# Kernel optimization log

Hardware: AMD Instinct MI355X
Metric: run time of the kernel (lower is better)

## Reference

```python
import jax, jax.numpy as jnp
import numpy as np
from jax import lax

B, T, D, H = 4, 2048, 1024, 8
DH = D // H          # head dim
K = 4                # causal conv kernel
DFF = int(D * 4 / 3) # 1365, GLU up-projection
EPS_LN = 1e-5
EPS_SLSTM = 1e-8


def layernorm(x, g, b):
    mu = jnp.mean(x, axis=-1, keepdims=True)
    var = jnp.mean(jnp.square(x - mu), axis=-1, keepdims=True)
    return (x - mu) * lax.rsqrt(var + EPS_LN) * g + b


def bd(x, W):
    # block-diagonal linear: x [..., D], W [H, DH, DH]
    xh = x.reshape(x.shape[:-1] + (H, DH))
    return jnp.einsum('...hd,hde->...he', xh, W).reshape(x.shape)


def _forward(x, Wz, Wi, Wf, Wo, bz, bi, bf, bo, Rz, Ri, Rf, Ro,
             conv_w, conv_b, ln_g, ln_b, gn_g, gn_b,
             left_w, left_b, right_w, right_b, last_w, last_b):
    x_norm = layernorm(x, ln_g, ln_b)
    # causal conv1d (pad left K-1), NCH layout
    xc = x_norm.transpose(0, 2, 1)
    conv = lax.conv_general_dilated(xc, conv_w, (1,), [(K - 1, 0)],
                                    dimension_numbers=('NCH', 'OIH', 'NCH'))
    conv = conv + conv_b[None, :, None]
    x_if = conv.transpose(0, 2, 1)
    x_if = x_if * jax.nn.sigmoid(x_if)  # swish (dropout = identity in eval)
    x_zo = x_norm

    # precompute input-side block-diagonal projections for all timesteps
    wz = bd(x_zo, Wz) + bz
    wi = bd(x_if, Wi) + bi
    wf = bd(x_if, Wf) + bf
    wo = bd(x_zo, Wo) + bo

    zeros = jnp.zeros((B, D), x.dtype)

    def step(carry, inp):
        h, c, n, m = carry
        wz_t, wi_t, wf_t, wo_t = inp
        z_bar = wz_t + bd(h, Rz)
        i_bar = wi_t + bd(h, Ri)
        f_bar = wf_t + bd(h, Rf)
        o_bar = wo_t + bd(h, Ro)
        z = jnp.tanh(z_bar)
        o = jax.nn.sigmoid(o_bar)
        m_next = jnp.maximum(f_bar + m, i_bar)
        i = jnp.exp(i_bar - m_next)
        f = jnp.exp(f_bar + m - m_next)
        c_next = f * c + i * z
        n_next = f * n + i
        h_next = o * (c_next / jnp.maximum(jnp.abs(n_next), EPS_SLSTM))
        return (h_next, c_next, n_next, m_next), h_next

    seq = (wz.transpose(1, 0, 2), wi.transpose(1, 0, 2),
           wf.transpose(1, 0, 2), wo.transpose(1, 0, 2))
    (h, c, n, m), hs = lax.scan(step, (zeros, zeros, zeros, zeros), seq)
    h_seq = hs.transpose(1, 0, 2)  # [B, T, D]

    h_gn = layernorm(h_seq, gn_g, gn_b)
    h_skip = h_gn + x
    hn = layernorm(h_skip, ln_g, ln_b)  # shared ln params, as in the module
    z_left = hn @ left_w.T + left_b
    z_right = jax.nn.gelu(hn @ right_w.T + right_b, approximate=False)
    out = (z_left * z_right) @ last_w.T + last_b + h_skip
    return out, h, c, n, m


def setup_inputs() -> dict:
    key = jax.random.key(0)
    ks = jax.random.split(key, 16)
    s = 0.02
    nrm = lambda k, shape: jax.random.normal(k, shape, jnp.float32) * s
    return dict(
        x=jax.random.normal(ks[0], (B, T, D), jnp.float32),
        Wz=nrm(ks[1], (H, DH, DH)), Wi=nrm(ks[2], (H, DH, DH)),
        Wf=nrm(ks[3], (H, DH, DH)), Wo=nrm(ks[4], (H, DH, DH)),
        bz=jnp.zeros(D), bi=jnp.zeros(D), bf=jnp.zeros(D), bo=jnp.zeros(D),
        Rz=nrm(ks[5], (H, DH, DH)), Ri=nrm(ks[6], (H, DH, DH)),
        Rf=nrm(ks[7], (H, DH, DH)), Ro=nrm(ks[8], (H, DH, DH)),
        conv_w=nrm(ks[9], (D, D, K)), conv_b=jnp.zeros(D),
        ln_g=jnp.ones(D), ln_b=jnp.zeros(D),
        gn_g=jnp.ones(D), gn_b=jnp.zeros(D),
        left_w=nrm(ks[10], (DFF, D)), left_b=jnp.zeros(DFF),
        right_w=nrm(ks[11], (DFF, D)), right_b=jnp.zeros(DFF),
        last_w=nrm(ks[12], (D, DFF)), last_b=jnp.zeros(D),
    )


def reference(x, Wz, Wi, Wf, Wo, bz, bi, bf, bo, Rz, Ri, Rf, Ro,
              conv_w, conv_b, ln_g, ln_b, gn_g, gn_b,
              left_w, left_b, right_w, right_b, last_w, last_b):
    out, h, c, n, m = _forward(x, Wz, Wi, Wf, Wo, bz, bi, bf, bo,
                               Rz, Ri, Rf, Ro, conv_w, conv_b,
                               ln_g, ln_b, gn_g, gn_b,
                               left_w, left_b, right_w, right_b,
                               last_w, last_b)
    return (out, (h, c, n, m))
```

## Files before the change

kernel.cpp:

```cpp
#include <hip/hip_runtime.h>

typedef unsigned short u16;
typedef unsigned int u32;
typedef __attribute__((ext_vector_type(8))) short short8;
typedef __attribute__((ext_vector_type(4))) float f32x4;

#define B_  4
#define T_  2048
#define D_  1024
#define H_  8
#define DH_ 128
#define DFF_ 1365
#define DFFP 1408
#define NLR 2816

__device__ __forceinline__ u16 f2bf(float f) {
    u32 u = __float_as_uint(f);
    u32 r = (u + 0x7fffu + ((u >> 16) & 1u)) >> 16;
    return (u16)r;
}
__device__ __forceinline__ float bf2f(u16 v) {
    return __uint_as_float(((u32)v) << 16);
}
__device__ __forceinline__ float frcp(float x) { return __builtin_amdgcn_rcpf(x); }

__global__ void ln_x_kernel(const float* __restrict__ x, const float* __restrict__ g,
                            const float* __restrict__ b, u16* __restrict__ xn) {
    int row = blockIdx.x, tid = threadIdx.x;
    int lane = tid & 63, wv = tid >> 6;
    __shared__ float red[8];
    float4 v = ((const float4*)(x + (size_t)row * D_))[tid];
    float s = v.x + v.y + v.z + v.w;
    float s2 = v.x * v.x + v.y * v.y + v.z * v.z + v.w * v.w;
#pragma unroll
    for (int o = 32; o >= 1; o >>= 1) { s += __shfl_xor(s, o); s2 += __shfl_xor(s2, o); }
    if (lane == 0) { red[wv] = s; red[4 + wv] = s2; }
    __syncthreads();
    s = red[0] + red[1] + red[2] + red[3];
    s2 = red[4] + red[5] + red[6] + red[7];
    float mu = s * (1.f / D_);
    float var = s2 * (1.f / D_) - mu * mu;
    float inv = rsqrtf(var + 1e-5f);
    int c0 = tid * 4;
    ushort4 o4;
    o4.x = f2bf((v.x - mu) * inv * g[c0 + 0] + b[c0 + 0]);
    o4.y = f2bf((v.y - mu) * inv * g[c0 + 1] + b[c0 + 1]);
    o4.z = f2bf((v.z - mu) * inv * g[c0 + 2] + b[c0 + 2]);
    o4.w = f2bf((v.w - mu) * inv * g[c0 + 3] + b[c0 + 3]);
    ((ushort4*)(xn + (size_t)row * D_))[tid] = o4;
}

__global__ void build_bconv2(const float* __restrict__ cw, u16* __restrict__ oh,
                             u16* __restrict__ ol) {
    int i = blockIdx.x * 256 + threadIdx.x;
    int din = i & 1023, kt = (i >> 10) & 3, dout = i >> 12;
    float v = cw[((size_t)dout * D_ + din) * 4 + kt];
    u16 hi = f2bf(v);
    oh[i] = hi;
    ol[i] = f2bf(v - bf2f(hi));
}

__global__ __launch_bounds__(256) void proj2_kernel(
    const u16* __restrict__ xn, const float* __restrict__ xif,
    const float* __restrict__ Wz, const float* __restrict__ Wi,
    const float* __restrict__ Wf, const float* __restrict__ Wo,
    const float* __restrict__ bz, const float* __restrict__ bi,
    const float* __restrict__ bfv, const float* __restrict__ bo,
    float* __restrict__ wgif, u16* __restrict__ wgzo) {
    const int m0 = blockIdx.x * 32;
    const int hd = blockIdx.y;
    const int tid = threadIdx.x;
    const int e = tid & 127, half = tid >> 7;
    __shared__ float xns[32][128];
    __shared__ float xfs[32][128];
    for (int s = tid; s < 32 * 128; s += 256) {
        int r = s >> 7, d = s & 127;
        xns[r][d] = bf2f(xn[(size_t)(m0 + r) * D_ + hd * DH_ + d]);
        xfs[r][d] = xif[(size_t)(m0 + r) * D_ + hd * DH_ + d];
    }
    __syncthreads();
    const float* WA = half ? Wo : Wz;
    const float* WB = half ? Wf : Wi;
    float accA[32], accB[32];
#pragma unroll
    for (int r = 0; r < 32; ++r) { accA[r] = 0.f; accB[r] = 0.f; }
    for (int d = 0; d < 128; ++d) {
        float wa = WA[((size_t)hd * DH_ + d) * DH_ + e];
        float wb = WB[((size_t)hd * DH_ + d) * DH_ + e];
#pragma unroll
        for (int r = 0; r < 32; ++r) {
            accA[r] += xns[r][d] * wa;
            accB[r] += xfs[r][d] * wb;
        }
    }
    float ba = half ? bo[hd * DH_ + e] : bz[hd * DH_ + e];
    float bb = half ? bfv[hd * DH_ + e] : bi[hd * DH_ + e];
#pragma unroll
    for (int r = 0; r < 32; ++r) {
        size_t base = ((size_t)(m0 + r) * D_ + hd * DH_ + e) * 2;
        wgif[base + half] = accB[r] + bb;
        wgzo[base + half] = f2bf(accA[r] + ba);
    }
}

__global__ void build_blr(const float* __restrict__ lw, const float* __restrict__ rw,
                          u16* __restrict__ o) {
    int i = blockIdx.x * 256 + threadIdx.x;
    int k = i & 1023, n = i >> 10;
    float v = 0.f;
    if (n < DFF_) v = lw[(size_t)n * D_ + k];
    else if (n >= DFFP && n < DFFP + DFF_) v = rw[(size_t)(n - DFFP) * D_ + k];
    o[i] = f2bf(v);
}
__global__ void build_blast(const float* __restrict__ lw, u16* __restrict__ o) {
    int n = blockIdx.x;
    for (int k = threadIdx.x; k < DFFP; k += 256) {
        float v = (k < DFF_) ? lw[(size_t)n * DFF_ + k] : 0.f;
        o[(size_t)n * DFFP + k] = f2bf(v);
    }
}

template <int MODE>
__global__ __launch_bounds__(256) void gemm_k(
    const u16* __restrict__ A, const u16* __restrict__ Bg, const u16* __restrict__ Bg2,
    int K, int lda,
    const float* __restrict__ bias0, const float* __restrict__ bias1,
    const float* __restrict__ add0, u16* __restrict__ o16, float* __restrict__ o32) {
    const int tid = threadIdx.x;
    const int m0 = blockIdx.y * 128;
    const int n0 = blockIdx.x * 128;
    __shared__ u16 As[128][72];
    __shared__ u16 Bs[128][72];
    __shared__ u16 Bs2[(MODE == 0) ? 128 : 1][72];

    f32x4 zero4 = {0.f, 0.f, 0.f, 0.f};
    f32x4 acc[4][4];
#pragma unroll
    for (int i = 0; i < 4; ++i)
#pragma unroll
        for (int j = 0; j < 4; ++j) acc[i][j] = zero4;

    const int lane = tid & 63, wv = tid >> 6;
    const int wr = (wv >> 1) * 64, wc = (wv & 1) * 64;
    const int fr = lane & 15, kg = (lane >> 4) * 8;

    for (int kb = 0; kb < K; kb += 64) {
#pragma unroll
        for (int it = 0; it < 4; ++it) {
            int slot = tid + it * 256;
            int r = slot >> 3, ch = slot & 7;
            uint4 va;
            if constexpr (MODE == 0) {
                int kk = kb + ch * 8;
                int ktap = kk >> 10, din = kk & 1023;
                int m = m0 + r;
                int t = m & (T_ - 1);
                if (t + ktap - 3 >= 0)
                    va = *(const uint4*)(A + (size_t)(m + ktap - 3) * D_ + din);
                else
                    va = make_uint4(0u, 0u, 0u, 0u);
            } else {
                va = *(const uint4*)(A + (size_t)(m0 + r) * lda + kb + ch * 8);
            }
            *(uint4*)(&As[r][ch * 8]) = va;
            uint4 vb = *(const uint4*)(Bg + (size_t)(n0 + r) * K + kb + ch * 8);
            *(uint4*)(&Bs[r][ch * 8]) = vb;
            if constexpr (MODE == 0) {
                uint4 vc = *(const uint4*)(Bg2 + (size_t)(n0 + r) * K + kb + ch * 8);
                *(uint4*)(&Bs2[r][ch * 8]) = vc;
            }
        }
        __syncthreads();
#pragma unroll
        for (int kt = 0; kt < 2; ++kt) {
            short8 af[4], bfr[4];
#pragma unroll
            for (int i = 0; i < 4; ++i)
                af[i] = *(const short8*)(&As[wr + i * 16 + fr][kt * 32 + kg]);
#pragma unroll
            for (int i = 0; i < 4; ++i)
                bfr[i] = *(const short8*)(&Bs[wc + i * 16 + fr][kt * 32 + kg]);
#pragma unroll
            for (int mi = 0; mi < 4; ++mi)
#pragma unroll
                for (int ni = 0; ni < 4; ++ni)
                    acc[mi][ni] = __builtin_amdgcn_mfma_f32_16x16x32_bf16(
                        af[mi], bfr[ni], acc[mi][ni], 0, 0, 0);
            if constexpr (MODE == 0) {
                short8 bl[4];
#pragma unroll
                for (int i = 0; i < 4; ++i)
                    bl[i] = *(const short8*)(&Bs2[wc + i * 16 + fr][kt * 32 + kg]);
#pragma unroll
                for (int mi = 0; mi < 4; ++mi)
#pragma unroll
                    for (int ni = 0; ni < 4; ++ni)
                        acc[mi][ni] = __builtin_amdgcn_mfma_f32_16x16x32_bf16(
                            af[mi], bl[ni], acc[mi][ni], 0, 0, 0);
            }
        }
        __syncthreads();
    }
#pragma unroll
    for (int mi = 0; mi < 4; ++mi) {
#pragma unroll
        for (int ni = 0; ni < 4; ++ni) {
#pragma unroll
            for (int r = 0; r < 4; ++r) {
                int row = m0 + wr + mi * 16 + (lane >> 4) * 4 + r;
                int col = n0 + wc + ni * 16 + fr;
                float v = acc[mi][ni][r];
                if constexpr (MODE == 0) {
                    float s = v + bias0[col];
                    float sw = s * frcp(1.f + __expf(-s));
                    o32[(size_t)row * D_ + col] = sw;
                } else if constexpr (MODE == 2) {
                    float bv = 0.f;
                    if (col < DFF_) bv = bias0[col];
                    else if (col >= DFFP && col < DFFP + DFF_) bv = bias1[col - DFFP];
                    o16[(size_t)row * NLR + col] = f2bf(v + bv);
                } else {
                    float r0 = v + bias0[col] + add0[(size_t)row * D_ + col];
                    o32[(size_t)row * D_ + col] = r0;
                }
            }
        }
    }
}

__global__ __launch_bounds__(512) void scan4_kernel(
    const float* __restrict__ wgif, const u16* __restrict__ wgzo,
    const float* __restrict__ Rz, const float* __restrict__ Ri,
    const float* __restrict__ Rf, const float* __restrict__ Ro,
    u16* __restrict__ hseq, float* __restrict__ st_out) {
    const int head = blockIdx.x;
    const int tid = threadIdx.x;
    const int lane = tid & 63, wv = tid >> 6;
    const int lc = lane & 15, lg = lane >> 4;

    __shared__ u16 hfH[2][4][64][8];
    __shared__ u16 hfL[2][4][64][8];
    __shared__ float zl[8][4][16][4];

    for (int i = tid; i < 2 * 4 * 64 * 8; i += 512) {
        ((u16*)hfH)[i] = 0;
        ((u16*)hfL)[i] = 0;
    }

    short8 bfh[4][4];
    short8 bfl[2][4];
    {
        const float* Rp[4] = {Rz, Ri, Rf, Ro};
        const int e = wv * 16 + lc;
#pragma unroll
        for (int g = 0; g < 4; ++g) {
            const float* R = Rp[g] + (size_t)head * DH_ * DH_;
#pragma unroll
            for (int kt = 0; kt < 4; ++kt) {
                short8 vh, vl;
#pragma unroll
                for (int j = 0; j < 8; ++j) {
                    int k = kt * 32 + lg * 8 + j;
                    float rv = R[(size_t)k * DH_ + e];
                    u16 hi = f2bf(rv);
                    vh[j] = (short)hi;
                    vl[j] = (short)f2bf(rv - bf2f(hi));
                }
                bfh[g][kt] = vh;
                if (g == 1) bfl[0][kt] = vl;
                if (g == 2) bfl[1][kt] = vl;
            }
        }
    }

    const int ab = lg;
    const int adq = wv * 16 + lc;
    const float* pifp = wgif + (((size_t)ab * T_) * D_ + head * DH_ + adq) * 2;
    const u16*  pzop = wgzo + (((size_t)ab * T_) * D_ + head * DH_ + adq) * 2;
    u16* hsp = hseq + ((size_t)ab * T_) * D_ + head * DH_ + adq;
    const int fpos = (((adq >> 5) * 64) + (((adq >> 3) & 3) * 16) + ab) * 8 + (adq & 7);
    const bool ard = (lc < 4);

    float c_s = 0.f, n_s = 0.f, m_s = 0.f, h_s = 0.f;
    float2 pif = *(const float2*)pifp; pifp += 2 * D_;
    u32 pzo = *(const u32*)pzop; pzop += 2 * D_;

    const short8 zero8 = {0, 0, 0, 0, 0, 0, 0, 0};
    __syncthreads();

    for (int t = 0; t < T_; ++t) {
        const int p = t & 1, q = p ^ 1;
        short8 ah[4], al[4];
#pragma unroll
        for (int kt = 0; kt < 4; ++kt) {
            ah[kt] = ard ? *(const short8*)(&hfH[p][kt][lane][0]) : zero8;
            al[kt] = ard ? *(const short8*)(&hfL[p][kt][lane][0]) : zero8;
        }
        f32x4 az = {0.f, 0.f, 0.f, 0.f}, ai = az, af2 = az, ao = az;
#pragma unroll
        for (int kt = 0; kt < 4; ++kt) {
            az  = __builtin_amdgcn_mfma_f32_16x16x32_bf16(ah[kt], bfh[0][kt], az, 0, 0, 0);
            ao  = __builtin_amdgcn_mfma_f32_16x16x32_bf16(ah[kt], bfh[3][kt], ao, 0, 0, 0);
            ai  = __builtin_amdgcn_mfma_f32_16x16x32_bf16(ah[kt], bfh[1][kt], ai, 0, 0, 0);
            af2 = __builtin_amdgcn_mfma_f32_16x16x32_bf16(ah[kt], bfh[2][kt], af2, 0, 0, 0);
        }
#pragma unroll
        for (int kt = 0; kt < 4; ++kt) {
            ai  = __builtin_amdgcn_mfma_f32_16x16x32_bf16(al[kt], bfh[1][kt], ai, 0, 0, 0);
            af2 = __builtin_amdgcn_mfma_f32_16x16x32_bf16(al[kt], bfh[2][kt], af2, 0, 0, 0);
        }
#pragma unroll
        for (int kt = 0; kt < 4; ++kt) {
            ai  = __builtin_amdgcn_mfma_f32_16x16x32_bf16(ah[kt], bfl[0][kt], ai, 0, 0, 0);
            af2 = __builtin_amdgcn_mfma_f32_16x16x32_bf16(ah[kt], bfl[1][kt], af2, 0, 0, 0);
        }
        if (lane < 16) {
            *(f32x4*)(&zl[wv][0][lc][0]) = az;
            *(f32x4*)(&zl[wv][1][lc][0]) = ai;
            *(f32x4*)(&zl[wv][2][lc][0]) = af2;
            *(f32x4*)(&zl[wv][3][lc][0]) = ao;
        }
        __builtin_amdgcn_sched_barrier(0);
        float gz = zl[wv][0][lc][ab];
        float gi = zl[wv][1][lc][ab];
        float gf = zl[wv][2][lc][ab];
        float go = zl[wv][3][lc][ab];
        float vz = bf2f((u16)(pzo & 0xffffu)) + gz;
        float vi = pif.x + gi;
        float vf = pif.y + gf;
        float vo = bf2f((u16)(pzo >> 16)) + go;
        if (t < T_ - 1) {
            pif = *(const float2*)pifp; pifp += 2 * D_;
            pzo = *(const u32*)pzop; pzop += 2 * D_;
        }
        float z = 1.f - 2.f * frcp(__expf(2.f * vz) + 1.f);
        float o = frcp(1.f + __expf(-vo));
        float mn = fmaxf(vf + m_s, vi);
        float ii = __expf(vi - mn);
        float ff = __expf(vf + m_s - mn);
        c_s = ff * c_s + ii * z;
        n_s = ff * n_s + ii;
        m_s = mn;
        h_s = o * c_s * frcp(fmaxf(fabsf(n_s), 1e-8f));
        u16 hb = f2bf(h_s);
        ((u16*)hfH)[q * 2048 + fpos] = hb;
        ((u16*)hfL)[q * 2048 + fpos] = f2bf(h_s - bf2f(hb));
        *hsp = hb; hsp += D_;
        asm volatile("s_waitcnt lgkmcnt(0)\n\ts_barrier" ::: "memory");
    }

    int pos = ab * D_ + head * DH_ + adq;
    st_out[pos] = h_s;
    st_out[4096 + pos] = c_s;
    st_out[8192 + pos] = n_s;
    st_out[12288 + pos] = m_s;
}

__global__ void post_kernel(const u16* __restrict__ hseq, const float* __restrict__ x,
                            const float* __restrict__ gn_g, const float* __restrict__ gn_b,
                            const float* __restrict__ ln_g, const float* __restrict__ ln_b,
                            float* __restrict__ hskip, u16* __restrict__ hn) {
    int row = blockIdx.x, tid = threadIdx.x;
    int lane = tid & 63, wv = tid >> 6;
    __shared__ float red[8];
    ushort4 hv = ((const ushort4*)(hseq + (size_t)row * D_))[tid];
    float h0 = bf2f(hv.x), h1 = bf2f(hv.y), h2 = bf2f(hv.z), h3 = bf2f(hv.w);
    float s = h0 + h1 + h2 + h3;
    float s2 = h0 * h0 + h1 * h1 + h2 * h2 + h3 * h3;
#pragma unroll
    for (int o = 32; o >= 1; o >>= 1) { s += __shfl_xor(s, o); s2 += __shfl_xor(s2, o); }
    if (lane == 0) { red[wv] = s; red[4 + wv] = s2; }
    __syncthreads();
    s = red[0] + red[1] + red[2] + red[3];
    s2 = red[4] + red[5] + red[6] + red[7];
    float mu = s * (1.f / D_);
    float var = s2 * (1.f / D_) - mu * mu;
    float inv = rsqrtf(var + 1e-5f);
    float4 xv = ((const float4*)(x + (size_t)row * D_))[tid];
    int c0 = tid * 4;
    float k0 = (h0 - mu) * inv * gn_g[c0 + 0] + gn_b[c0 + 0] + xv.x;
    float k1 = (h1 - mu) * inv * gn_g[c0 + 1] + gn_b[c0 + 1] + xv.y;
    float k2 = (h2 - mu) * inv * gn_g[c0 + 2] + gn_b[c0 + 2] + xv.z;
    float k3 = (h3 - mu) * inv * gn_g[c0 + 3] + gn_b[c0 + 3] + xv.w;
    ((float4*)(hskip + (size_t)row * D_))[tid] = make_float4(k0, k1, k2, k3);
    float t1 = k0 + k1 + k2 + k3;
    float t2 = k0 * k0 + k1 * k1 + k2 * k2 + k3 * k3;
#pragma unroll
    for (int o = 32; o >= 1; o >>= 1) { t1 += __shfl_xor(t1, o); t2 += __shfl_xor(t2, o); }
    __syncthreads();
    if (lane == 0) { red[wv] = t1; red[4 + wv] = t2; }
    __syncthreads();
    t1 = red[0] + red[1] + red[2] + red[3];
    t2 = red[4] + red[5] + red[6] + red[7];
    float mu2 = t1 * (1.f / D_);
    float var2 = t2 * (1.f / D_) - mu2 * mu2;
    float inv2 = rsqrtf(var2 + 1e-5f);
    ushort4 o4;
    o4.x = f2bf((k0 - mu2) * inv2 * ln_g[c0 + 0] + ln_b[c0 + 0]);
    o4.y = f2bf((k1 - mu2) * inv2 * ln_g[c0 + 1] + ln_b[c0 + 1]);
    o4.z = f2bf((k2 - mu2) * inv2 * ln_g[c0 + 2] + ln_b[c0 + 2]);
    o4.w = f2bf((k3 - mu2) * inv2 * ln_g[c0 + 3] + ln_b[c0 + 3]);
    ((ushort4*)(hn + (size_t)row * D_))[tid] = o4;
}

__global__ void glu_kernel(const u16* __restrict__ zlr, u16* __restrict__ glu) {
    int row = blockIdx.x;
    for (int n = threadIdx.x; n < DFFP; n += 256) {
        float g = 0.f;
        if (n < DFF_) {
            float zl = bf2f(zlr[(size_t)row * NLR + n]);
            float zr = bf2f(zlr[(size_t)row * NLR + DFFP + n]);
            float ge = 0.5f * zr * (1.f + erff(zr * 0.70710678118654752f));
            g = zl * ge;
        }
        glu[(size_t)row * DFFP + n] = f2bf(g);
    }
}

extern "C" void kernel_launch(void* const* d_in, const int* in_sizes, int n_in,
                              void* d_out, int out_size, void* d_ws, size_t ws_size,
                              hipStream_t stream) {
    const float* x      = (const float*)d_in[0];
    const float* Wz     = (const float*)d_in[1];
    const float* Wi     = (const float*)d_in[2];
    const float* Wf     = (const float*)d_in[3];
    const float* Wo     = (const float*)d_in[4];
    const float* bz     = (const float*)d_in[5];
    const float* bi     = (const float*)d_in[6];
    const float* bfb    = (const float*)d_in[7];
    const float* bo     = (const float*)d_in[8];
    const float* Rz     = (const float*)d_in[9];
    const float* Ri     = (const float*)d_in[10];
    const float* Rf     = (const float*)d_in[11];
    const float* Ro     = (const float*)d_in[12];
    const float* conv_w = (const float*)d_in[13];
    const float* conv_b = (const float*)d_in[14];
    const float* ln_g   = (const float*)d_in[15];
    const float* ln_b   = (const float*)d_in[16];
    const float* gn_g   = (const float*)d_in[17];
    const float* gn_b   = (const float*)d_in[18];
    const float* left_w = (const float*)d_in[19];
    const float* left_b = (const float*)d_in[20];
    const float* right_w= (const float*)d_in[21];
    const float* right_b= (const float*)d_in[22];
    const float* last_w = (const float*)d_in[23];
    const float* last_b = (const float*)d_in[24];

    char* ws = (char*)d_ws;
    u16*  BCH   = (u16*)(ws);
    u16*  BCL   = (u16*)(ws + 8388608);
    u16*  BLR   = (u16*)(ws + 16777216);
    u16*  BLAST = (u16*)(ws + 22544384);
    u16*  XN    = (u16*)(ws + 25427968);
    float* XIF32= (float*)(ws + 42205184);
    float* WGIF = (float*)(ws + 75759616);
    u16*  WGZO  = (u16*)(ws + 142868480);
    u16*  HSEQ  = (u16*)(ws);
    float* HSKIP= (float*)(ws + 42205184);
    u16*  HN    = (u16*)(ws + 25427968);
    u16*  ZLR   = (u16*)(ws + 75759616);
    u16*  GLU   = (u16*)(ws + 142868480);

    float* out = (float*)d_out;
    float* st_out = out + (size_t)B_ * T_ * D_;

    const int M = B_ * T_;

    ln_x_kernel<<<M, 256, 0, stream>>>(x, ln_g, ln_b, XN);
    build_bconv2<<<16384, 256, 0, stream>>>(conv_w, BCH, BCL);
    build_blr<<<11264, 256, 0, stream>>>(left_w, right_w, BLR);
    build_blast<<<1024, 256, 0, stream>>>(last_w, BLAST);

    gemm_k<0><<<dim3(8, 64), 256, 0, stream>>>(XN, BCH, BCL, 4096, D_, conv_b, nullptr,
                                               nullptr, nullptr, XIF32);
    proj2_kernel<<<dim3(256, 8), 256, 0, stream>>>(XN, XIF32, Wz, Wi, Wf, Wo,
                                                   bz, bi, bfb, bo, WGIF, WGZO);
    scan4_kernel<<<8, 512, 0, stream>>>(WGIF, WGZO, Rz, Ri, Rf, Ro, HSEQ, st_out);
    post_kernel<<<M, 256, 0, stream>>>(HSEQ, x, gn_g, gn_b, ln_g, ln_b, HSKIP, HN);
    gemm_k<2><<<dim3(22, 64), 256, 0, stream>>>(HN, BLR, nullptr, 1024, 1024,
                                                left_b, right_b, nullptr, ZLR, nullptr);
    glu_kernel<<<M, 256, 0, stream>>>(ZLR, GLU);
    gemm_k<3><<<dim3(8, 64), 256, 0, stream>>>(GLU, BLAST, nullptr, DFFP, DFFP,
                                               last_b, nullptr, HSKIP, nullptr, out);
}
```

Before: 2.710 ms.

## Replicate h across MFMA rows to drop LDS gate exchange in scan

The recurrent scan kernel now loads the h vector into every MFMA row group (replicated A operand), so each lane can pick its own gate result directly from the accumulator instead of staging results through the zl shared buffer. This removes the per-step LDS write/read round trip and the lane-16 predicate. It also splits the hi/lo correction MFMAs into independent accumulators to shorten dependency chains, unrolls the time loop by two, and prefetches the input projections two steps ahead. The cost is more accumulator registers and redundant MFMA rows.

Result: faster. 2.580 ms (-4.8%).

```diff
diff --git a/kernel.cpp b/kernel.cpp
--- a/kernel.cpp
+++ b/kernel.cpp
@@ -228,7 +228,7 @@
     }
 }
 
-__global__ __launch_bounds__(512) void scan4_kernel(
+__global__ __launch_bounds__(512) void scan5_kernel(
     const float* __restrict__ wgif, const u16* __restrict__ wgzo,
     const float* __restrict__ Rz, const float* __restrict__ Ri,
     const float* __restrict__ Rf, const float* __restrict__ Ro,
@@ -238,11 +238,10 @@
     const int lane = tid & 63, wv = tid >> 6;
     const int lc = lane & 15, lg = lane >> 4;
 
-    __shared__ u16 hfH[2][4][64][8];
-    __shared__ u16 hfL[2][4][64][8];
-    __shared__ float zl[8][4][16][4];
-
-    for (int i = tid; i < 2 * 4 * 64 * 8; i += 512) {
+    __shared__ u16 hfH[2][4][16][8];
+    __shared__ u16 hfL[2][4][16][8];
+
+    for (int i = tid; i < 2 * 4 * 16 * 8; i += 512) {
         ((u16*)hfH)[i] = 0;
         ((u16*)hfL)[i] = 0;
     }
@@ -278,75 +277,74 @@
     const float* pifp = wgif + (((size_t)ab * T_) * D_ + head * DH_ + adq) * 2;
     const u16*  pzop = wgzo + (((size_t)ab * T_) * D_ + head * DH_ + adq) * 2;
     u16* hsp = hseq + ((size_t)ab * T_) * D_ + head * DH_ + adq;
-    const int fpos = (((adq >> 5) * 64) + (((adq >> 3) & 3) * 16) + ab) * 8 + (adq & 7);
-    const bool ard = (lc < 4);
+    const int wpos = ((adq >> 5) * 16 + (ab * 4 + ((adq >> 3) & 3))) * 8 + (adq & 7);
+    const int rbase = ((lc & 3) * 4 + lg) * 8;
 
     float c_s = 0.f, n_s = 0.f, m_s = 0.f, h_s = 0.f;
-    float2 pif = *(const float2*)pifp; pifp += 2 * D_;
-    u32 pzo = *(const u32*)pzop; pzop += 2 * D_;
-
-    const short8 zero8 = {0, 0, 0, 0, 0, 0, 0, 0};
-    __syncthreads();
-
-    for (int t = 0; t < T_; ++t) {
-        const int p = t & 1, q = p ^ 1;
-        short8 ah[4], al[4];
-#pragma unroll
-        for (int kt = 0; kt < 4; ++kt) {
-            ah[kt] = ard ? *(const short8*)(&hfH[p][kt][lane][0]) : zero8;
-            al[kt] = ard ? *(const short8*)(&hfL[p][kt][lane][0]) : zero8;
-        }
-        f32x4 az = {0.f, 0.f, 0.f, 0.f}, ai = az, af2 = az, ao = az;
-#pragma unroll
-        for (int kt = 0; kt < 4; ++kt) {
-            az  = __builtin_amdgcn_mfma_f32_16x16x32_bf16(ah[kt], bfh[0][kt], az, 0, 0, 0);
-            ao  = __builtin_amdgcn_mfma_f32_16x16x32_bf16(ah[kt], bfh[3][kt], ao, 0, 0, 0);
-            ai  = __builtin_amdgcn_mfma_f32_16x16x32_bf16(ah[kt], bfh[1][kt], ai, 0, 0, 0);
-            af2 = __builtin_amdgcn_mfma_f32_16x16x32_bf16(ah[kt], bfh[2][kt], af2, 0, 0, 0);
-        }
-#pragma unroll
-        for (int kt = 0; kt < 4; ++kt) {
-            ai  = __builtin_amdgcn_mfma_f32_16x16x32_bf16(al[kt], bfh[1][kt], ai, 0, 0, 0);
-            af2 = __builtin_amdgcn_mfma_f32_16x16x32_bf16(al[kt], bfh[2][kt], af2, 0, 0, 0);
-        }
-#pragma unroll
-        for (int kt = 0; kt < 4; ++kt) {
-            ai  = __builtin_amdgcn_mfma_f32_16x16x32_bf16(ah[kt], bfl[0][kt], ai, 0, 0, 0);
-            af2 = __builtin_amdgcn_mfma_f32_16x16x32_bf16(ah[kt], bfl[1][kt], af2, 0, 0, 0);
-        }
-        if (lane < 16) {
-            *(f32x4*)(&zl[wv][0][lc][0]) = az;
-            *(f32x4*)(&zl[wv][1][lc][0]) = ai;
-            *(f32x4*)(&zl[wv][2][lc][0]) = af2;
-            *(f32x4*)(&zl[wv][3][lc][0]) = ao;
-        }
-        __builtin_amdgcn_sched_barrier(0);
-        float gz = zl[wv][0][lc][ab];
-        float gi = zl[wv][1][lc][ab];
-        float gf = zl[wv][2][lc][ab];
-        float go = zl[wv][3][lc][ab];
-        float vz = bf2f((u16)(pzo & 0xffffu)) + gz;
-        float vi = pif.x + gi;
-        float vf = pif.y + gf;
-        float vo = bf2f((u16)(pzo >> 16)) + go;
-        if (t < T_ - 1) {
-            pif = *(const float2*)pifp; pifp += 2 * D_;
-            pzo = *(const u32*)pzop; pzop += 2 * D_;
-        }
-        float z = 1.f - 2.f * frcp(__expf(2.f * vz) + 1.f);
-        float o = frcp(1.f + __expf(-vo));
-        float mn = fmaxf(vf + m_s, vi);
-        float ii = __expf(vi - mn);
-        float ff = __expf(vf + m_s - mn);
-        c_s = ff * c_s + ii * z;
-        n_s = ff * n_s + ii;
-        m_s = mn;
-        h_s = o * c_s * frcp(fmaxf(fabsf(n_s), 1e-8f));
-        u16 hb = f2bf(h_s);
-        ((u16*)hfH)[q * 2048 + fpos] = hb;
-        ((u16*)hfL)[q * 2048 + fpos] = f2bf(h_s - bf2f(hb));
-        *hsp = hb; hsp += D_;
-        asm volatile("s_waitcnt lgkmcnt(0)\n\ts_barrier" ::: "memory");
+    float2 pif0 = *(const float2*)pifp;
+    u32 pzo0 = *(const u32*)pzop;
+    float2 pif1 = *(const float2*)(pifp + 2 * D_);
+    u32 pzo1 = *(const u32*)(pzop + 2 * D_);
+
+    __syncthreads();
+
+    for (int t = 0; t < T_; t += 2) {
+#pragma unroll
+        for (int half = 0; half < 2; ++half) {
+            const int p = half, q = half ^ 1;
+            const int tc = t + half;
+            float2 cif = half ? pif1 : pif0;
+            u32 czo = half ? pzo1 : pzo0;
+            if (tc + 2 < T_) {
+                const float2* fi = (const float2*)(pifp + (size_t)(tc + 2) * 2 * D_);
+                const u32* fz = (const u32*)(pzop + (size_t)(tc + 2) * 2 * D_);
+                if (half) { pif1 = *fi; pzo1 = *fz; }
+                else      { pif0 = *fi; pzo0 = *fz; }
+            }
+            short8 ah[4], al[4];
+#pragma unroll
+            for (int kt = 0; kt < 4; ++kt) {
+                ah[kt] = *(const short8*)(&((u16*)hfH)[p * 512 + kt * 128 + rbase]);
+                al[kt] = *(const short8*)(&((u16*)hfL)[p * 512 + kt * 128 + rbase]);
+            }
+            f32x4 zz = {0.f, 0.f, 0.f, 0.f};
+            f32x4 oo = zz, i1 = zz, i2 = zz, i3 = zz, f1 = zz, ff2 = zz, f3 = zz;
+#pragma unroll
+            for (int kt = 0; kt < 4; ++kt) {
+                zz = __builtin_amdgcn_mfma_f32_16x16x32_bf16(ah[kt], bfh[0][kt], zz, 0, 0, 0);
+                oo = __builtin_amdgcn_mfma_f32_16x16x32_bf16(ah[kt], bfh[3][kt], oo, 0, 0, 0);
+                i1 = __builtin_amdgcn_mfma_f32_16x16x32_bf16(ah[kt], bfh[1][kt], i1, 0, 0, 0);
+                f1 = __builtin_amdgcn_mfma_f32_16x16x32_bf16(ah[kt], bfh[2][kt], f1, 0, 0, 0);
+                i2 = __builtin_amdgcn_mfma_f32_16x16x32_bf16(al[kt], bfh[1][kt], i2, 0, 0, 0);
+                ff2 = __builtin_amdgcn_mfma_f32_16x16x32_bf16(al[kt], bfh[2][kt], ff2, 0, 0, 0);
+                i3 = __builtin_amdgcn_mfma_f32_16x16x32_bf16(ah[kt], bfl[0][kt], i3, 0, 0, 0);
+                f3 = __builtin_amdgcn_mfma_f32_16x16x32_bf16(ah[kt], bfl[1][kt], f3, 0, 0, 0);
+            }
+            f32x4 ii4 = (i1 + i2) + i3;
+            f32x4 ff4 = (f1 + ff2) + f3;
+            float gz = (lg == 0) ? zz[0] : (lg == 1) ? zz[1] : (lg == 2) ? zz[2] : zz[3];
+            float gi = (lg == 0) ? ii4[0] : (lg == 1) ? ii4[1] : (lg == 2) ? ii4[2] : ii4[3];
+            float gf = (lg == 0) ? ff4[0] : (lg == 1) ? ff4[1] : (lg == 2) ? ff4[2] : ff4[3];
+            float go = (lg == 0) ? oo[0] : (lg == 1) ? oo[1] : (lg == 2) ? oo[2] : oo[3];
+            float vz = bf2f((u16)(czo & 0xffffu)) + gz;
+            float vi = cif.x + gi;
+            float vf = cif.y + gf;
+            float vo = bf2f((u16)(czo >> 16)) + go;
+            float z = 1.f - 2.f * frcp(__expf(2.f * vz) + 1.f);
+            float o = frcp(1.f + __expf(-vo));
+            float mn = fmaxf(vf + m_s, vi);
+            float ii = __expf(vi - mn);
+            float ff = __expf(vf + m_s - mn);
+            c_s = ff * c_s + ii * z;
+            n_s = ff * n_s + ii;
+            m_s = mn;
+            h_s = o * c_s * frcp(fmaxf(fabsf(n_s), 1e-8f));
+            u16 hb = f2bf(h_s);
+            ((u16*)hfH)[q * 512 + wpos] = hb;
+            ((u16*)hfL)[q * 512 + wpos] = f2bf(h_s - bf2f(hb));
+            *hsp = hb; hsp += D_;
+            asm volatile("s_waitcnt lgkmcnt(0)\n\ts_barrier" ::: "memory");
+        }
     }
 
     int pos = ab * D_ + head * DH_ + adq;
@@ -475,7 +473,7 @@
                                                nullptr, nullptr, XIF32);
     proj2_kernel<<<dim3(256, 8), 256, 0, stream>>>(XN, XIF32, Wz, Wi, Wf, Wo,
                                                    bz, bi, bfb, bo, WGIF, WGZO);
-    scan4_kernel<<<8, 512, 0, stream>>>(WGIF, WGZO, Rz, Ri, Rf, Ro, HSEQ, st_out);
+    scan5_kernel<<<8, 512, 0, stream>>>(WGIF, WGZO, Rz, Ri, Rf, Ro, HSEQ, st_out);
     post_kernel<<<M, 256, 0, stream>>>(HSEQ, x, gn_g, gn_b, ln_g, ln_b, HSKIP, HN);
     gemm_k<2><<<dim3(22, 64), 256, 0, stream>>>(HN, BLR, nullptr, 1024, 1024,
                                                 left_b, right_b, nullptr, ZLR, nullptr);
```
